# Optimization experiments

Measured on AMD Instinct MI355X. Metric: run time of the kernel, lower is better.

The kernel has to match this reference:

```python
import jax, jax.numpy as jnp
import numpy as np

N, C, H, W = 1, 1, 4096, 4096

def setup_inputs() -> dict:
    key = jax.random.key(0)
    x = jax.random.normal(key, (N, C, H, W), dtype=jnp.float32)
    return {"x": x}

def reference(x):
    # torch.median returns the lower of the two middle values for even counts:
    # take the k-th smallest with k = (n-1)//2.
    n = x.size
    median = jnp.sort(x.reshape(-1))[(n - 1) // 2]
    # threshold everything below the median to zero
    thresholded = jnp.where(x < median, jnp.float32(0.0), x)
    # 7x7 max pool, stride 1, padding 3 (torch pads with -inf for max pool)
    pooled = jax.lax.reduce_window(
        thresholded,
        -jnp.inf,
        jax.lax.max,
        window_dimensions=(1, 1, 7, 7),
        window_strides=(1, 1, 1, 1),
        padding=[(0, 0), (0, 0), (3, 3), (3, 3)],
    )
    # In the original, gather(flatten(thresholded), max_indices) == pooled,
    # so binarize where the thresholded value equals its local window max.
    binarized = jnp.where(thresholded == pooled, jnp.float32(1.0), jnp.float32(0.0))
    return binarized * x
```

## Files before the change

kernel.cpp:

```cpp
#include <hip/hip_runtime.h>
#include <math.h>

#define IMG_H 4096
#define IMG_W 4096
#define TS 64
#define HALO 3
#define TW 70
#define THS 71
#define HMS 65
#define NBINS 4096
#define CBLK 1024
#define CAPB 4096
#define WLO (-0.001953125f)
#define WHI ( 0.001953125f)
#define MCAP 1024
#define NSUB 2048

struct SelState { float median; };

__device__ __forceinline__ unsigned f2u(float f) {
    unsigned b = __float_as_uint(f);
    unsigned mask = (unsigned)(-(int)(b >> 31)) | 0x80000000u;
    return b ^ mask;
}
__device__ __forceinline__ float u2f(unsigned u) {
    unsigned mask = (u >> 31) ? 0x80000000u : 0xFFFFFFFFu;
    return __uint_as_float(u ^ mask);
}

__device__ __forceinline__ int val_bin(float v) {
    float t = (v + 4.0f) * 512.0f;
    int b = (int)t;
    b = b < 0 ? 0 : b;
    b = b > (NBINS - 1) ? (NBINS - 1) : b;
    return b;
}

__device__ __forceinline__ int sub_bin(float v) {
    float t = (v - WLO) * (float)(NSUB * 256);
    int b = (int)t;
    b = b < 0 ? 0 : b;
    b = b > (NSUB - 1) ? (NSUB - 1) : b;
    return b;
}

__global__ __launch_bounds__(512, 8) void count_compact(
    const float4* __restrict__ x4, int n4,
    unsigned* __restrict__ belowCnt,
    unsigned* __restrict__ candCnt,
    unsigned* __restrict__ candA)
{
    __shared__ unsigned buf[CAPB];
    __shared__ unsigned wred[8];
    __shared__ unsigned lcnt;
    const int t = threadIdx.x;
    if (t == 0) lcnt = 0;
    __syncthreads();

    unsigned below = 0;
    const int idx = blockIdx.x * 512 + t;
    const int stride = CBLK * 512;

    if (n4 == 8 * stride) {
        float4 v[8];
        #pragma unroll
        for (int j = 0; j < 8; j++) v[j] = x4[idx + j * stride];
        #pragma unroll
        for (int j = 0; j < 8; j++) {
            float vs[4] = {v[j].x, v[j].y, v[j].z, v[j].w};
            #pragma unroll
            for (int u = 0; u < 4; u++) {
                float vv = vs[u];
                below += (vv < WLO) ? 1u : 0u;
                if (vv >= WLO && vv < WHI) {
                    unsigned p = atomicAdd(&lcnt, 1u);
                    if (p < CAPB) buf[p] = f2u(vv);
                }
            }
        }
    } else {
        for (int i = idx; i < n4; i += stride) {
            float4 v = x4[i];
            float vs[4] = {v.x, v.y, v.z, v.w};
            #pragma unroll
            for (int u = 0; u < 4; u++) {
                float vv = vs[u];
                below += (vv < WLO) ? 1u : 0u;
                if (vv >= WLO && vv < WHI) {
                    unsigned p = atomicAdd(&lcnt, 1u);
                    if (p < CAPB) buf[p] = f2u(vv);
                }
            }
        }
    }

    #pragma unroll
    for (int off = 32; off >= 1; off >>= 1) below += __shfl_down(below, off, 64);
    if ((t & 63) == 0) wred[t >> 6] = below;
    __syncthreads();
    if (t == 0) {
        unsigned tot = 0;
        #pragma unroll
        for (int w = 0; w < 8; w++) tot += wred[w];
        belowCnt[blockIdx.x] = tot;
        candCnt[blockIdx.x] = lcnt;
    }
    unsigned m = lcnt; if (m > CAPB) m = CAPB;
    const unsigned gbase = (unsigned)blockIdx.x * CAPB;
    for (unsigned i = t; i < m; i += 512) candA[gbase + i] = buf[i];
}

__global__ __launch_bounds__(1024) void finalize_fb(
    const float4* __restrict__ x4, int n4, unsigned K,
    const unsigned* __restrict__ belowCnt,
    const unsigned* __restrict__ candCnt,
    const unsigned* __restrict__ candA,
    unsigned* __restrict__ candB,
    SelState* __restrict__ st)
{
    __shared__ unsigned hist[NSUB];
    __shared__ unsigned mem[MCAP];
    __shared__ unsigned lh[NBINS];
    __shared__ unsigned ccs[CBLK];
    __shared__ unsigned wsA[16], wsB[16], wsC[16];
    __shared__ unsigned s_below, s_M, s_ovf, s_sb, s_kr2, mcnt;
    __shared__ unsigned s_bin, s_krem, s_m, s_pref, s_kr;
    const int t = threadIdx.x;
    const unsigned lane = t & 63, wid = t >> 6;

    const unsigned rbase = wid * 64u;
    unsigned key[64];
    #pragma unroll
    for (int g = 0; g < 64; g++)
        key[g] = candA[(rbase + (unsigned)g) * CAPB + lane];

    {
        const unsigned cc = candCnt[t];
        ccs[t] = cc;
        unsigned bsum = belowCnt[t];
        unsigned csum = cc;
        unsigned osum = (cc > CAPB) ? 1u : 0u;
        #pragma unroll
        for (int off = 32; off >= 1; off >>= 1) {
            bsum += __shfl_down(bsum, off, 64);
            csum += __shfl_down(csum, off, 64);
            osum += __shfl_down(osum, off, 64);
        }
        if (lane == 0) { wsA[wid] = bsum; wsB[wid] = csum; wsC[wid] = osum; }
        if (t == 0) mcnt = 0;
        for (int i = t; i < NSUB; i += 1024) hist[i] = 0;
        __syncthreads();
        if (t == 0) {
            unsigned b = 0, c = 0, o = 0;
            #pragma unroll
            for (int w = 0; w < 16; w++) { b += wsA[w]; c += wsB[w]; o += wsC[w]; }
            s_below = b; s_M = c; s_ovf = o;
        }
        __syncthreads();
    }

    const unsigned below = s_below, M = s_M;
    bool resolved = false;
    if (s_ovf == 0u && K >= below && (K - below) < M) {
        const unsigned kRem = K - below;

        #pragma unroll
        for (int g = 0; g < 64; g++)
            if (lane < ccs[rbase + (unsigned)g])
                atomicAdd(&hist[sub_bin(u2f(key[g]))], 1u);
        for (int r = t; r < CBLK; r += 1024) {
            const unsigned cc = ccs[r];
            for (unsigned j = 64; j < cc; j++)
                atomicAdd(&hist[sub_bin(u2f(candA[(unsigned)r * CAPB + j]))], 1u);
        }
        __syncthreads();

        unsigned d0 = hist[t * 2], d1 = hist[t * 2 + 1];
        unsigned loc2 = d0 + d1;
        unsigned s2 = loc2;
        #pragma unroll
        for (int off = 1; off < 64; off <<= 1) {
            unsigned u = __shfl_up(s2, off, 64);
            if (lane >= off) s2 += u;
        }
        if (lane == 63) wsA[wid] = s2;
        __syncthreads();
        unsigned base2 = 0;
        for (unsigned w = 0; w < wid; w++) base2 += wsA[w];
        unsigned excl2 = base2 + s2 - loc2;
        if (kRem >= excl2 && kRem < excl2 + loc2) {
            if (kRem < excl2 + d0) { s_sb = (unsigned)(t * 2);     s_kr2 = kRem - excl2; }
            else                   { s_sb = (unsigned)(t * 2 + 1); s_kr2 = kRem - excl2 - d0; }
        }
        __syncthreads();

        const int sb = (int)s_sb;
        #pragma unroll
        for (int g = 0; g < 64; g++) {
            if (lane < ccs[rbase + (unsigned)g] &&
                sub_bin(u2f(key[g])) == sb) {
                unsigned p = atomicAdd(&mcnt, 1u);
                if (p < MCAP) mem[p] = key[g];
            }
        }
        for (int r = t; r < CBLK; r += 1024) {
            const unsigned cc = ccs[r];
            for (unsigned j = 64; j < cc; j++) {
                unsigned k2 = candA[(unsigned)r * CAPB + j];
                if (sub_bin(u2f(k2)) == sb) {
                    unsigned p = atomicAdd(&mcnt, 1u);
                    if (p < MCAP) mem[p] = k2;
                }
            }
        }
        __syncthreads();
        if (mcnt <= MCAP) {
            const unsigned m = mcnt, kr2 = s_kr2;
            if ((unsigned)t < m) {
                unsigned ku = mem[t], c = 0, e = 0;
                for (unsigned j = 0; j < m; j++) {
                    unsigned kj = mem[j];
                    c += (kj < ku);
                    e += (kj == ku);
                }
                if (c <= kr2 && kr2 < c + e) st->median = u2f(ku);
            }
            resolved = true;
        }
    }
    if (resolved) return;

    __syncthreads();
    for (int i = t; i < NBINS; i += 1024) lh[i] = 0;
    __syncthreads();
    for (int i = t; i < n4; i += 1024) {
        float4 v = x4[i];
        atomicAdd(&lh[val_bin(v.x)], 1u);
        atomicAdd(&lh[val_bin(v.y)], 1u);
        atomicAdd(&lh[val_bin(v.z)], 1u);
        atomicAdd(&lh[val_bin(v.w)], 1u);
    }
    __syncthreads();

    {
        unsigned cb[4];
        unsigned local = 0;
        #pragma unroll
        for (int j = 0; j < 4; j++) { cb[j] = lh[t * 4 + j]; local += cb[j]; }
        unsigned s = local;
        #pragma unroll
        for (int off = 1; off < 64; off <<= 1) {
            unsigned u = __shfl_up(s, off, 64);
            if (lane >= off) s += u;
        }
        if (lane == 63) wsA[wid] = s;
        __syncthreads();
        unsigned base = 0;
        for (unsigned w = 0; w < wid; w++) base += wsA[w];
        unsigned excl = base + s - local;
        if (K >= excl && K < excl + local) {
            unsigned cum = excl;
            #pragma unroll
            for (int j = 0; j < 4; j++) {
                if (K < cum + cb[j]) { s_bin = (unsigned)(t * 4 + j); s_krem = K - cum; break; }
                cum += cb[j];
            }
        }
        if (t == 0) s_m = 0;
        __syncthreads();
    }

    {
        const int b = (int)s_bin;
        for (int i = t; i < n4; i += 1024) {
            float4 v = x4[i];
            float vs[4] = {v.x, v.y, v.z, v.w};
            #pragma unroll
            for (int j = 0; j < 4; j++) {
                if (val_bin(vs[j]) == b) {
                    unsigned p = atomicAdd(&s_m, 1u);
                    candB[p] = f2u(vs[j]);
                }
            }
        }
        __syncthreads();
    }

    const int M2 = (int)s_m;
    if (t == 0) { s_pref = 0; s_kr = s_krem; }
    for (int p = 0; p < 3; p++) {
        const int shift = (p == 0) ? 21 : ((p == 1) ? 10 : 0);
        const int bits  = (p == 2) ? 10 : 11;
        const int nb    = 1 << bits;
        for (int i = t; i < nb; i += 1024) lh[i] = 0;
        __syncthreads();
        const unsigned pref = s_pref;
        for (int i = t; i < M2; i += 1024) {
            unsigned u = candB[i];
            bool ok = (p == 0) || ((u >> ((p == 1) ? 21 : 10)) == pref);
            if (ok) atomicAdd(&lh[(u >> shift) & (unsigned)(nb - 1)], 1u);
        }
        __syncthreads();
        const int P = nb >> 10;
        unsigned c0 = lh[t * (P ? P : 1)];
        unsigned c1 = (P == 2) ? lh[t * 2 + 1] : 0u;
        if (P == 0) { c0 = (t < nb) ? lh[t] : 0u; c1 = 0u; }
        unsigned local = c0 + c1;
        unsigned s = local;
        #pragma unroll
        for (int off = 1; off < 64; off <<= 1) {
            unsigned u = __shfl_up(s, off, 64);
            if (lane >= off) s += u;
        }
        if (lane == 63) wsA[wid] = s;
        __syncthreads();
        unsigned base = 0;
        for (unsigned w = 0; w < wid; w++) base += wsA[w];
        unsigned excl = base + s - local;
        unsigned kRem2 = s_kr;
        __syncthreads();
        if (kRem2 >= excl && kRem2 < excl + local) {
            if (P == 2) {
                if (kRem2 < excl + c0) { s_pref = (pref << bits) | (unsigned)(t * 2);     s_kr = kRem2 - excl; }
                else                  { s_pref = (pref << bits) | (unsigned)(t * 2 + 1); s_kr = kRem2 - excl - c0; }
            } else {
                s_pref = (pref << bits) | (unsigned)t;
                s_kr = kRem2 - excl;
            }
        }
        __syncthreads();
    }
    if (t == 0) st->median = u2f(s_pref);
}

__global__ __launch_bounds__(512) void nms_kernel(
    const float* __restrict__ x, float* __restrict__ out,
    const SelState* __restrict__ st)
{
    __shared__ float th[TW * THS];
    __shared__ float hm[TW * HMS];

    const float med = st->median;
    const float NEGINF = -__builtin_inff();
    const int bx = blockIdx.x, by = blockIdx.y;
    const int gy0 = by * TS - HALO;
    const int gcol0 = bx * TS - 4;

    if (bx >= 1 && bx <= (IMG_W / TS) - 2 && by >= 1 && by <= (IMG_H / TS) - 2) {
        #pragma unroll
        for (int k = 0; k < 3; k++) {
            int task = threadIdx.x + k * 512;
            if (task < TW * 18) {
                int r = task / 18, q = task - r * 18;
                const float4 v = *(const float4*)&x[(gy0 + r) * IMG_W + (gcol0 + q * 4)];
                float vs[4] = {v.x, v.y, v.z, v.w};
                #pragma unroll
                for (int cmp = 0; cmp < 4; cmp++) {
                    int c = q * 4 - 1 + cmp;
                    if ((unsigned)c < (unsigned)TW)
                        th[r * THS + c] = (vs[cmp] < med) ? 0.0f : vs[cmp];
                }
            }
        }
    } else {
        for (int task = threadIdx.x; task < TW * 18; task += 512) {
            int r = task / 18, q = task - r * 18;
            int gy = gy0 + r;
            int gxb = gcol0 + q * 4;
            bool rowok = (gy >= 0 && gy < IMG_H);
            float vs[4];
            if (rowok && gxb >= 0 && gxb + 4 <= IMG_W) {
                float4 v = *(const float4*)&x[gy * IMG_W + gxb];
                vs[0] = v.x; vs[1] = v.y; vs[2] = v.z; vs[3] = v.w;
            } else if (rowok) {
                #pragma unroll
                for (int cmp = 0; cmp < 4; cmp++) {
                    int gx = gxb + cmp;
                    vs[cmp] = (gx >= 0 && gx < IMG_W) ? x[gy * IMG_W + gx] : NEGINF;
                }
            } else {
                vs[0] = vs[1] = vs[2] = vs[3] = NEGINF;
            }
            #pragma unroll
            for (int cmp = 0; cmp < 4; cmp++) {
                int c = q * 4 - 1 + cmp;
                if ((unsigned)c < (unsigned)TW) {
                    float v = vs[cmp];
                    v = (v == NEGINF) ? v : ((v < med) ? 0.0f : v);
                    th[r * THS + c] = v;
                }
            }
        }
    }
    __syncthreads();

    for (int task = threadIdx.x; task < TW * 8; task += 512) {
        int r = task % TW;
        int c0 = (task / TW) * 8;
        float w[7];
        #pragma unroll
        for (int i = 0; i < 14; i++) {
            w[i % 7] = th[r * THS + c0 + i];
            if (i >= 6) {
                float m = w[0];
                #pragma unroll
                for (int k = 1; k < 7; k++) m = fmaxf(m, w[k]);
                hm[r * HMS + c0 + i - 6] = m;
            }
        }
    }
    __syncthreads();

    {
        const int c = threadIdx.x & 63;
        const int rr0 = (threadIdx.x >> 6) * 8;
        float w[7];
        #pragma unroll
        for (int i = 0; i < 14; i++) {
            w[i % 7] = hm[(rr0 + i) * HMS + c];
            if (i >= 6) {
                int R = rr0 + i - 6;
                float m = w[0];
                #pragma unroll
                for (int k = 1; k < 7; k++) m = fmaxf(m, w[k]);
                float t = th[(R + HALO) * THS + (c + HALO)];
                int gy = by * TS + R;
                int gx = bx * TS + c;
                float o = 0.0f;
                if (t == m) {
                    o = (t != 0.0f) ? t : x[gy * IMG_W + gx];
                }
                out[gy * IMG_W + gx] = o;
            }
        }
    }
}

extern "C" void kernel_launch(void* const* d_in, const int* in_sizes, int n_in,
                              void* d_out, int out_size, void* d_ws, size_t ws_size,
                              hipStream_t stream)
{
    const float* x = (const float*)d_in[0];
    float* out = (float*)d_out;
    const int n = in_sizes[0];
    const unsigned K = (unsigned)((n - 1) / 2);

    char* ws = (char*)d_ws;
    SelState* st       = (SelState*)ws;
    unsigned* belowCnt = (unsigned*)(ws + 1024);
    unsigned* candCnt  = (unsigned*)(ws + 1024 + 4096);
    unsigned* candA    = (unsigned*)(ws + ws_size / 2);

    const int n4 = n / 4;
    count_compact<<<CBLK, 512, 0, stream>>>((const float4*)x, n4,
                                            belowCnt, candCnt, candA);
    finalize_fb<<<1, 1024, 0, stream>>>((const float4*)x, n4, K,
                                        belowCnt, candCnt, candA,
                                        (unsigned*)d_out, st);
    dim3 fg(IMG_W / TS, IMG_H / TS);
    nms_kernel<<<fg, 512, 0, stream>>>(x, out, st);
}
```

Measured before the change: 146.6 us.

## Fuse median selection and NMS into one cooperative persistent kernel with grid syncs

Replaces the three launches (count/compact, single-block finalize, tiled NMS) with a single cooperative kernel of 512 blocks. Grid syncs separate the phases. The candidate histogram and sub-bin selection are spread across all blocks using global atomics instead of one 1024-thread block. Each block then processes 8 NMS tiles in a persistent loop. This removes the serial single-block finalize bottleneck and the launch gaps, at the cost of grid-sync overhead, fewer resident blocks for the NMS phase, and a redundant O(m^2) rank computation run in every block.

```diff
diff --git a/kernel.cpp b/kernel.cpp
--- a/kernel.cpp
+++ b/kernel.cpp
@@ -1,5 +1,8 @@
 #include <hip/hip_runtime.h>
+#include <hip/hip_cooperative_groups.h>
 #include <math.h>
+
+namespace cg = cooperative_groups;
 
 #define IMG_H 4096
 #define IMG_W 4096
@@ -9,13 +12,16 @@
 #define THS 71
 #define HMS 65
 #define NBINS 4096
-#define CBLK 1024
+#define GRIDB 512
+#define NTHR 512
 #define CAPB 4096
 #define WLO (-0.001953125f)
 #define WHI ( 0.001953125f)
 #define MCAP 1024
 #define NSUB 2048
 
+#define CBLK 1024
+
 struct SelState { float median; };
 
 __device__ __forceinline__ unsigned f2u(float f) {
@@ -27,7 +33,6 @@
     unsigned mask = (u >> 31) ? 0x80000000u : 0xFFFFFFFFu;
     return __uint_as_float(u ^ mask);
 }
-
 __device__ __forceinline__ int val_bin(float v) {
     float t = (v + 4.0f) * 512.0f;
     int b = (int)t;
@@ -35,7 +40,6 @@
     b = b > (NBINS - 1) ? (NBINS - 1) : b;
     return b;
 }
-
 __device__ __forceinline__ int sub_bin(float v) {
     float t = (v - WLO) * (float)(NSUB * 256);
     int b = (int)t;
@@ -44,10 +48,352 @@
     return b;
 }
 
+union SMem {
+    struct { unsigned buf[CAPB]; unsigned wred[8]; unsigned lcnt; } a;
+    struct { unsigned lh[NBINS];
+             unsigned s_below, s_M, s_ovf, s_sb, s_kr2, s_cnt;
+             unsigned s_bin, s_krem, s_m, s_pref, s_kr;
+             float s_med; } b;
+    struct { float th[TW * THS]; float hm[TW * HMS]; } c;
+};
+
+__global__ __launch_bounds__(NTHR, 4) void fused_nms(
+    const float4* __restrict__ x4, int n4, unsigned K,
+    const float* __restrict__ x, float* __restrict__ out,
+    unsigned* __restrict__ candB,
+    SelState* __restrict__ st,
+    unsigned* __restrict__ belowCnt,
+    unsigned* __restrict__ candCnt,
+    unsigned* __restrict__ candA,
+    unsigned* __restrict__ ghist,
+    unsigned* __restrict__ gmem,
+    unsigned* __restrict__ gmcnt, unsigned* __restrict__ gfb)
+{
+    __shared__ SMem sm;
+    cg::grid_group grid = cg::this_grid();
+    const int t = threadIdx.x;
+    const int b = blockIdx.x;
+    const unsigned lane = t & 63, wid = t >> 6;
+
+    if (t == 0) sm.a.lcnt = 0;
+    __syncthreads();
+    if (b == 0) {
+        for (int i = t; i < NSUB; i += NTHR) ghist[i] = 0;
+        if (t == 0) { *gmcnt = 0; *gfb = 0; }
+    }
+    unsigned below = 0;
+    const int gid = b * NTHR + t;
+    const int stride = GRIDB * NTHR;
+    if (n4 == 16 * stride) {
+        #pragma unroll
+        for (int half = 0; half < 2; half++) {
+            float4 v[8];
+            #pragma unroll
+            for (int j = 0; j < 8; j++) v[j] = x4[gid + (half * 8 + j) * stride];
+            #pragma unroll
+            for (int j = 0; j < 8; j++) {
+                float vs[4] = {v[j].x, v[j].y, v[j].z, v[j].w};
+                #pragma unroll
+                for (int u = 0; u < 4; u++) {
+                    float vv = vs[u];
+                    below += (vv < WLO) ? 1u : 0u;
+                    if (vv >= WLO && vv < WHI) {
+                        unsigned p = atomicAdd(&sm.a.lcnt, 1u);
+                        if (p < CAPB) sm.a.buf[p] = f2u(vv);
+                    }
+                }
+            }
+        }
+    } else {
+        for (int i = gid; i < n4; i += stride) {
+            float4 v = x4[i];
+            float vs[4] = {v.x, v.y, v.z, v.w};
+            #pragma unroll
+            for (int u = 0; u < 4; u++) {
+                float vv = vs[u];
+                below += (vv < WLO) ? 1u : 0u;
+                if (vv >= WLO && vv < WHI) {
+                    unsigned p = atomicAdd(&sm.a.lcnt, 1u);
+                    if (p < CAPB) sm.a.buf[p] = f2u(vv);
+                }
+            }
+        }
+    }
+    #pragma unroll
+    for (int off = 32; off >= 1; off >>= 1) below += __shfl_down(below, off, 64);
+    if (lane == 0) sm.a.wred[wid] = below;
+    __syncthreads();
+    if (t == 0) {
+        unsigned tot = 0;
+        #pragma unroll
+        for (int w = 0; w < 8; w++) tot += sm.a.wred[w];
+        belowCnt[b] = tot;
+        candCnt[b] = sm.a.lcnt;
+    }
+    unsigned m0 = sm.a.lcnt; if (m0 > CAPB) m0 = CAPB;
+    for (unsigned i = t; i < m0; i += NTHR) candA[(unsigned)b * CAPB + i] = sm.a.buf[i];
+    grid.sync();
+
+    {
+        const unsigned ccv = candCnt[t];
+        unsigned bsum = belowCnt[t];
+        unsigned csum = ccv;
+        unsigned osum = (ccv > CAPB) ? 1u : 0u;
+        #pragma unroll
+        for (int off = 32; off >= 1; off >>= 1) {
+            bsum += __shfl_down(bsum, off, 64);
+            csum += __shfl_down(csum, off, 64);
+            osum += __shfl_down(osum, off, 64);
+        }
+        if (lane == 0) { sm.b.lh[wid] = bsum; sm.b.lh[8 + wid] = csum; sm.b.lh[16 + wid] = osum; }
+        __syncthreads();
+        if (t == 0) {
+            unsigned bb = 0, cc = 0, oo = 0;
+            #pragma unroll
+            for (int w = 0; w < 8; w++) { bb += sm.b.lh[w]; cc += sm.b.lh[8 + w]; oo += sm.b.lh[16 + w]; }
+            sm.b.s_below = bb; sm.b.s_M = cc; sm.b.s_ovf = oo;
+        }
+        __syncthreads();
+    }
+    {
+        unsigned cc = candCnt[b]; if (cc > CAPB) cc = CAPB;
+        for (unsigned j = t; j < cc; j += NTHR)
+            atomicAdd(&ghist[sub_bin(u2f(candA[(unsigned)b * CAPB + j]))], 1u);
+    }
+    grid.sync();
+
+    const unsigned belowT = sm.b.s_below, Mtot = sm.b.s_M;
+    const bool fastok = (sm.b.s_ovf == 0u) && (K >= belowT) && (K - belowT < Mtot);
+    if (fastok) {
+        const unsigned kRem = K - belowT;
+        unsigned d[4], local = 0;
+        #pragma unroll
+        for (int j = 0; j < 4; j++) { d[j] = ghist[t * 4 + j]; local += d[j]; }
+        unsigned s = local;
+        #pragma unroll
+        for (int off = 1; off < 64; off <<= 1) {
+            unsigned u = __shfl_up(s, off, 64);
+            if (lane >= off) s += u;
+        }
+        if (lane == 63) sm.b.lh[wid] = s;
+        __syncthreads();
+        unsigned base = 0;
+        for (unsigned w = 0; w < wid; w++) base += sm.b.lh[w];
+        unsigned excl = base + s - local;
+        if (kRem >= excl && kRem < excl + local) {
+            unsigned cum = excl;
+            #pragma unroll
+            for (int j = 0; j < 4; j++) {
+                if (kRem < cum + d[j]) {
+                    sm.b.s_sb = (unsigned)(t * 4 + j);
+                    sm.b.s_kr2 = kRem - cum;
+                    sm.b.s_cnt = d[j];
+                    break;
+                }
+                cum += d[j];
+            }
+        }
+        __syncthreads();
+    }
+    bool needfb = true;
+    if (fastok) needfb = (sm.b.s_cnt > MCAP);
+    if (!needfb) {
+        unsigned cc = candCnt[b]; if (cc > CAPB) cc = CAPB;
+        const unsigned sb = sm.b.s_sb;
+        for (unsigned j = t; j < cc; j += NTHR) {
+            unsigned key = candA[(unsigned)b * CAPB + j];
+            if ((unsigned)sub_bin(u2f(key)) == sb) {
+                unsigned p = atomicAdd(gmcnt, 1u);
+                if (p < MCAP) gmem[p] = key;
+            }
+        }
+    } else if (b == 0) {
+        for (int i = t; i < NBINS; i += NTHR) sm.b.lh[i] = 0;
+        __syncthreads();
+        for (int i = t; i < n4; i += NTHR) {
+            float4 v = x4[i];
+            atomicAdd(&sm.b.lh[val_bin(v.x)], 1u);
+            atomicAdd(&sm.b.lh[val_bin(v.y)], 1u);
+            atomicAdd(&sm.b.lh[val_bin(v.z)], 1u);
+            atomicAdd(&sm.b.lh[val_bin(v.w)], 1u);
+        }
+        __syncthreads();
+        if (t == 0) {
+            unsigned cum = 0;
+            for (int i = 0; i < NBINS; i++) {
+                unsigned c = sm.b.lh[i];
+                if (K < cum + c) { sm.b.s_bin = (unsigned)i; sm.b.s_krem = K - cum; break; }
+                cum += c;
+            }
+            sm.b.s_m = 0;
+        }
+        __syncthreads();
+        {
+            const unsigned bin = sm.b.s_bin;
+            for (int i = t; i < n4; i += NTHR) {
+                float4 v = x4[i];
+                float vs[4] = {v.x, v.y, v.z, v.w};
+                #pragma unroll
+                for (int j = 0; j < 4; j++) {
+                    if ((unsigned)val_bin(vs[j]) == bin) {
+                        unsigned p = atomicAdd(&sm.b.s_m, 1u);
+                        candB[p] = f2u(vs[j]);
+                    }
+                }
+            }
+            __syncthreads();
+        }
+        const int M2 = (int)sm.b.s_m;
+        if (t == 0) { sm.b.s_pref = 0; sm.b.s_kr = sm.b.s_krem; }
+        __syncthreads();
+        for (int p = 0; p < 3; p++) {
+            const int shift = (p == 0) ? 21 : ((p == 1) ? 10 : 0);
+            const int bits  = (p == 2) ? 10 : 11;
+            const int nb    = 1 << bits;
+            for (int i = t; i < nb; i += NTHR) sm.b.lh[i] = 0;
+            __syncthreads();
+            const unsigned pref = sm.b.s_pref;
+            for (int i = t; i < M2; i += NTHR) {
+                unsigned u = candB[i];
+                bool ok = (p == 0) || ((u >> ((p == 1) ? 21 : 10)) == pref);
+                if (ok) atomicAdd(&sm.b.lh[(u >> shift) & (unsigned)(nb - 1)], 1u);
+            }
+            __syncthreads();
+            if (t == 0) {
+                unsigned kr = sm.b.s_kr, cum = 0;
+                for (int i = 0; i < nb; i++) {
+                    unsigned c = sm.b.lh[i];
+                    if (kr < cum + c) { sm.b.s_pref = (pref << bits) | (unsigned)i; sm.b.s_kr = kr - cum; break; }
+                    cum += c;
+                }
+            }
+            __syncthreads();
+        }
+        if (t == 0) { st->median = u2f(sm.b.s_pref); *gfb = 1u; }
+    }
+    grid.sync();
+
+    float med;
+    if (*gfb) {
+        med = st->median;
+    } else {
+        const unsigned m = *gmcnt;
+        const unsigned kr2 = sm.b.s_kr2;
+        for (unsigned tt = t; tt < m; tt += NTHR) {
+            unsigned ku = gmem[tt], c = 0, e = 0;
+            for (unsigned j = 0; j < m; j++) {
+                unsigned kj = gmem[j];
+                c += (kj < ku);
+                e += (kj == ku);
+            }
+            if (c <= kr2 && kr2 < c + e) sm.b.s_med = u2f(ku);
+        }
+        __syncthreads();
+        med = sm.b.s_med;
+    }
+
+    const float NEGINF = -__builtin_inff();
+    for (int it = 0; it < 8; ++it) {
+        __syncthreads();
+        const int tile = b * 8 + it;
+        const int bx = tile & 63, by = tile >> 6;
+        const int gy0 = by * TS - HALO;
+        const int gcol0 = bx * TS - 4;
+
+        if (bx >= 1 && bx <= 62 && by >= 1 && by <= 62) {
+            #pragma unroll
+            for (int k = 0; k < 3; k++) {
+                int task = t + k * NTHR;
+                if (task < TW * 18) {
+                    int r = task / 18, q = task - r * 18;
+                    const float4 v = *(const float4*)&x[(gy0 + r) * IMG_W + (gcol0 + q * 4)];
+                    float vs[4] = {v.x, v.y, v.z, v.w};
+                    #pragma unroll
+                    for (int cmp = 0; cmp < 4; cmp++) {
+                        int c = q * 4 - 1 + cmp;
+                        if ((unsigned)c < (unsigned)TW)
+                            sm.c.th[r * THS + c] = (vs[cmp] < med) ? 0.0f : vs[cmp];
+                    }
+                }
+            }
+        } else {
+            for (int task = t; task < TW * 18; task += NTHR) {
+                int r = task / 18, q = task - r * 18;
+                int gy = gy0 + r;
+                int gxb = gcol0 + q * 4;
+                bool rowok = (gy >= 0 && gy < IMG_H);
+                float vs[4];
+                if (rowok && gxb >= 0 && gxb + 4 <= IMG_W) {
+                    float4 v = *(const float4*)&x[gy * IMG_W + gxb];
+                    vs[0] = v.x; vs[1] = v.y; vs[2] = v.z; vs[3] = v.w;
+                } else if (rowok) {
+                    #pragma unroll
+                    for (int cmp = 0; cmp < 4; cmp++) {
+                        int gx = gxb + cmp;
+                        vs[cmp] = (gx >= 0 && gx < IMG_W) ? x[gy * IMG_W + gx] : NEGINF;
+                    }
+                } else {
+                    vs[0] = vs[1] = vs[2] = vs[3] = NEGINF;
+                }
+                #pragma unroll
+                for (int cmp = 0; cmp < 4; cmp++) {
+                    int c = q * 4 - 1 + cmp;
+                    if ((unsigned)c < (unsigned)TW) {
+                        float v = vs[cmp];
+                        v = (v == NEGINF) ? v : ((v < med) ? 0.0f : v);
+                        sm.c.th[r * THS + c] = v;
+                    }
+                }
+            }
+        }
+        __syncthreads();
+
+        for (int task = t; task < TW * 8; task += NTHR) {
+            int r = task % TW;
+            int c0 = (task / TW) * 8;
+            float w[7];
+            #pragma unroll
+            for (int i = 0; i < 14; i++) {
+                w[i % 7] = sm.c.th[r * THS + c0 + i];
+                if (i >= 6) {
+                    float m = w[0];
+                    #pragma unroll
+                    for (int k = 1; k < 7; k++) m = fmaxf(m, w[k]);
+                    sm.c.hm[r * HMS + c0 + i - 6] = m;
+                }
+            }
+        }
+        __syncthreads();
+
+        {
+            const int c = t & 63;
+            const int rr0 = (t >> 6) * 8;
+            float w[7];
+            #pragma unroll
+            for (int i = 0; i < 14; i++) {
+                w[i % 7] = sm.c.hm[(rr0 + i) * HMS + c];
+                if (i >= 6) {
+                    int R = rr0 + i - 6;
+                    float m = w[0];
+                    #pragma unroll
+                    for (int k = 1; k < 7; k++) m = fmaxf(m, w[k]);
+                    float tv = sm.c.th[(R + HALO) * THS + (c + HALO)];
+                    int gy = by * TS + R;
+                    int gx = bx * TS + c;
+                    float o = 0.0f;
+                    if (tv == m) {
+                        o = (tv != 0.0f) ? tv : x[gy * IMG_W + gx];
+                    }
+                    out[gy * IMG_W + gx] = o;
+                }
+            }
+        }
+    }
+}
+
 __global__ __launch_bounds__(512, 8) void count_compact(
     const float4* __restrict__ x4, int n4,
-    unsigned* __restrict__ belowCnt,
-    unsigned* __restrict__ candCnt,
+    unsigned* __restrict__ belowCnt, unsigned* __restrict__ candCnt,
     unsigned* __restrict__ candA)
 {
     __shared__ unsigned buf[CAPB];
@@ -56,44 +402,22 @@
     const int t = threadIdx.x;
     if (t == 0) lcnt = 0;
     __syncthreads();
-
     unsigned below = 0;
     const int idx = blockIdx.x * 512 + t;
     const int stride = CBLK * 512;
-
-    if (n4 == 8 * stride) {
-        float4 v[8];
-        #pragma unroll
-        for (int j = 0; j < 8; j++) v[j] = x4[idx + j * stride];
-        #pragma unroll
-        for (int j = 0; j < 8; j++) {
-            float vs[4] = {v[j].x, v[j].y, v[j].z, v[j].w};
-            #pragma unroll
-            for (int u = 0; u < 4; u++) {
-                float vv = vs[u];
-                below += (vv < WLO) ? 1u : 0u;
-                if (vv >= WLO && vv < WHI) {
-                    unsigned p = atomicAdd(&lcnt, 1u);
-                    if (p < CAPB) buf[p] = f2u(vv);
-                }
-            }
-        }
-    } else {
-        for (int i = idx; i < n4; i += stride) {
-            float4 v = x4[i];
-            float vs[4] = {v.x, v.y, v.z, v.w};
-            #pragma unroll
-            for (int u = 0; u < 4; u++) {
-                float vv = vs[u];
-                below += (vv < WLO) ? 1u : 0u;
-                if (vv >= WLO && vv < WHI) {
-                    unsigned p = atomicAdd(&lcnt, 1u);
-                    if (p < CAPB) buf[p] = f2u(vv);
-                }
-            }
-        }
-    }
-
+    for (int i = idx; i < n4; i += stride) {
+        float4 v = x4[i];
+        float vs[4] = {v.x, v.y, v.z, v.w};
+        #pragma unroll
+        for (int u = 0; u < 4; u++) {
+            float vv = vs[u];
+            below += (vv < WLO) ? 1u : 0u;
+            if (vv >= WLO && vv < WHI) {
+                unsigned p = atomicAdd(&lcnt, 1u);
+                if (p < CAPB) buf[p] = f2u(vv);
+            }
+        }
+    }
     #pragma unroll
     for (int off = 32; off >= 1; off >>= 1) below += __shfl_down(below, off, 64);
     if ((t & 63) == 0) wred[t >> 6] = below;
@@ -112,10 +436,8 @@
 
 __global__ __launch_bounds__(1024) void finalize_fb(
     const float4* __restrict__ x4, int n4, unsigned K,
-    const unsigned* __restrict__ belowCnt,
-    const unsigned* __restrict__ candCnt,
-    const unsigned* __restrict__ candA,
-    unsigned* __restrict__ candB,
+    const unsigned* __restrict__ belowCnt, const unsigned* __restrict__ candCnt,
+    const unsigned* __restrict__ candA, unsigned* __restrict__ candB,
     SelState* __restrict__ st)
 {
     __shared__ unsigned hist[NSUB];
@@ -127,13 +449,11 @@
     __shared__ unsigned s_bin, s_krem, s_m, s_pref, s_kr;
     const int t = threadIdx.x;
     const unsigned lane = t & 63, wid = t >> 6;
-
     const unsigned rbase = wid * 64u;
     unsigned key[64];
     #pragma unroll
     for (int g = 0; g < 64; g++)
         key[g] = candA[(rbase + (unsigned)g) * CAPB + lane];
-
     {
         const unsigned cc = candCnt[t];
         ccs[t] = cc;
@@ -151,19 +471,17 @@
         for (int i = t; i < NSUB; i += 1024) hist[i] = 0;
         __syncthreads();
         if (t == 0) {
-            unsigned b = 0, c = 0, o = 0;
-            #pragma unroll
-            for (int w = 0; w < 16; w++) { b += wsA[w]; c += wsB[w]; o += wsC[w]; }
-            s_below = b; s_M = c; s_ovf = o;
-        }
-        __syncthreads();
-    }
-
+            unsigned bb = 0, cc2 = 0, oo = 0;
+            #pragma unroll
+            for (int w = 0; w < 16; w++) { bb += wsA[w]; cc2 += wsB[w]; oo += wsC[w]; }
+            s_below = bb; s_M = cc2; s_ovf = oo;
+        }
+        __syncthreads();
+    }
     const unsigned below = s_below, M = s_M;
     bool resolved = false;
     if (s_ovf == 0u && K >= below && (K - below) < M) {
         const unsigned kRem = K - below;
-
         #pragma unroll
         for (int g = 0; g < 64; g++)
             if (lane < ccs[rbase + (unsigned)g])
@@ -174,7 +492,6 @@
                 atomicAdd(&hist[sub_bin(u2f(candA[(unsigned)r * CAPB + j]))], 1u);
         }
         __syncthreads();
-
         unsigned d0 = hist[t * 2], d1 = hist[t * 2 + 1];
         unsigned loc2 = d0 + d1;
         unsigned s2 = loc2;
@@ -193,12 +510,10 @@
             else                   { s_sb = (unsigned)(t * 2 + 1); s_kr2 = kRem - excl2 - d0; }
         }
         __syncthreads();
-
         const int sb = (int)s_sb;
         #pragma unroll
         for (int g = 0; g < 64; g++) {
-            if (lane < ccs[rbase + (unsigned)g] &&
-                sub_bin(u2f(key[g])) == sb) {
+            if (lane < ccs[rbase + (unsigned)g] && sub_bin(u2f(key[g])) == sb) {
                 unsigned p = atomicAdd(&mcnt, 1u);
                 if (p < MCAP) mem[p] = key[g];
             }
@@ -229,7 +544,6 @@
         }
     }
     if (resolved) return;
-
     __syncthreads();
     for (int i = t; i < NBINS; i += 1024) lh[i] = 0;
     __syncthreads();
@@ -241,7 +555,6 @@
         atomicAdd(&lh[val_bin(v.w)], 1u);
     }
     __syncthreads();
-
     {
         unsigned cb[4];
         unsigned local = 0;
@@ -269,15 +582,14 @@
         if (t == 0) s_m = 0;
         __syncthreads();
     }
-
     {
-        const int b = (int)s_bin;
+        const int bb = (int)s_bin;
         for (int i = t; i < n4; i += 1024) {
             float4 v = x4[i];
             float vs[4] = {v.x, v.y, v.z, v.w};
             #pragma unroll
             for (int j = 0; j < 4; j++) {
-                if (val_bin(vs[j]) == b) {
+                if (val_bin(vs[j]) == bb) {
                     unsigned p = atomicAdd(&s_m, 1u);
                     candB[p] = f2u(vs[j]);
                 }
@@ -285,7 +597,6 @@
         }
         __syncthreads();
     }
-
     const int M2 = (int)s_m;
     if (t == 0) { s_pref = 0; s_kr = s_krem; }
     for (int p = 0; p < 3; p++) {
@@ -322,7 +633,7 @@
         if (kRem2 >= excl && kRem2 < excl + local) {
             if (P == 2) {
                 if (kRem2 < excl + c0) { s_pref = (pref << bits) | (unsigned)(t * 2);     s_kr = kRem2 - excl; }
-                else                  { s_pref = (pref << bits) | (unsigned)(t * 2 + 1); s_kr = kRem2 - excl - c0; }
+                else                   { s_pref = (pref << bits) | (unsigned)(t * 2 + 1); s_kr = kRem2 - excl - c0; }
             } else {
                 s_pref = (pref << bits) | (unsigned)t;
                 s_kr = kRem2 - excl;
@@ -339,14 +650,12 @@
 {
     __shared__ float th[TW * THS];
     __shared__ float hm[TW * HMS];
-
     const float med = st->median;
     const float NEGINF = -__builtin_inff();
     const int bx = blockIdx.x, by = blockIdx.y;
     const int gy0 = by * TS - HALO;
     const int gcol0 = bx * TS - 4;
-
-    if (bx >= 1 && bx <= (IMG_W / TS) - 2 && by >= 1 && by <= (IMG_H / TS) - 2) {
+    if (bx >= 1 && bx <= 62 && by >= 1 && by <= 62) {
         #pragma unroll
         for (int k = 0; k < 3; k++) {
             int task = threadIdx.x + k * 512;
@@ -393,7 +702,6 @@
         }
     }
     __syncthreads();
-
     for (int task = threadIdx.x; task < TW * 8; task += 512) {
         int r = task % TW;
         int c0 = (task / TW) * 8;
@@ -410,7 +718,6 @@
         }
     }
     __syncthreads();
-
     {
         const int c = threadIdx.x & 63;
         const int rr0 = (threadIdx.x >> 6) * 8;
@@ -423,12 +730,12 @@
                 float m = w[0];
                 #pragma unroll
                 for (int k = 1; k < 7; k++) m = fmaxf(m, w[k]);
-                float t = th[(R + HALO) * THS + (c + HALO)];
+                float tv = th[(R + HALO) * THS + (c + HALO)];
                 int gy = by * TS + R;
                 int gx = bx * TS + c;
                 float o = 0.0f;
-                if (t == m) {
-                    o = (t != 0.0f) ? t : x[gy * IMG_W + gx];
+                if (tv == m) {
+                    o = (tv != 0.0f) ? tv : x[gy * IMG_W + gx];
                 }
                 out[gy * IMG_W + gx] = o;
             }
@@ -444,19 +751,34 @@
     float* out = (float*)d_out;
     const int n = in_sizes[0];
     const unsigned K = (unsigned)((n - 1) / 2);
-
     char* ws = (char*)d_ws;
+
     SelState* st       = (SelState*)ws;
-    unsigned* belowCnt = (unsigned*)(ws + 1024);
-    unsigned* candCnt  = (unsigned*)(ws + 1024 + 4096);
+    unsigned* gfb      = (unsigned*)(ws + 64);
+    unsigned* gmcnt    = (unsigned*)(ws + 128);
+    unsigned* ghist    = (unsigned*)(ws + 256);
+    unsigned* belowCnt = (unsigned*)(ws + 16384);
+    unsigned* candCnt  = (unsigned*)(ws + 24576);
+    unsigned* gmem     = (unsigned*)(ws + 32768);
     unsigned* candA    = (unsigned*)(ws + ws_size / 2);
 
-    const int n4 = n / 4;
-    count_compact<<<CBLK, 512, 0, stream>>>((const float4*)x, n4,
-                                            belowCnt, candCnt, candA);
-    finalize_fb<<<1, 1024, 0, stream>>>((const float4*)x, n4, K,
-                                        belowCnt, candCnt, candA,
-                                        (unsigned*)d_out, st);
-    dim3 fg(IMG_W / TS, IMG_H / TS);
-    nms_kernel<<<fg, 512, 0, stream>>>(x, out, st);
-}
+    const float4* x4 = (const float4*)x;
+    unsigned* candB = (unsigned*)d_out;
+    int n4 = n / 4;
+    unsigned Kv = K;
+
+    void* args[] = { (void*)&x4, (void*)&n4, (void*)&Kv, (void*)&x, (void*)&out,
+                     (void*)&candB, (void*)&st, (void*)&belowCnt, (void*)&candCnt,
+                     (void*)&candA, (void*)&ghist, (void*)&gmem, (void*)&gmcnt,
+                     (void*)&gfb };
+    hipError_t err = hipLaunchCooperativeKernel((void*)fused_nms,
+                                                dim3(GRIDB), dim3(NTHR),
+                                                args, 0, stream);
+    if (err != hipSuccess) {
+        count_compact<<<CBLK, 512, 0, stream>>>(x4, n4, belowCnt, candCnt, candA);
+        finalize_fb<<<1, 1024, 0, stream>>>(x4, n4, K, belowCnt, candCnt, candA,
+                                            candB, st);
+        dim3 fg(IMG_W / TS, IMG_H / TS);
+        nms_kernel<<<fg, 512, 0, stream>>>(x, out, st);
+    }
+}
```

Result: slower. 319.9 us (+118.2%).

## Fuse median counting and finalize into one kernel via last-block election

Applied to the files above, without the earlier changes.

Merges the count/compact kernel and the single-block finalize kernel into one launch. Each block increments a global done counter after a threadfence, and the last block to arrive runs the median selection with 512 threads instead of 1024. This removes one kernel launch and the gap between launches, but adds a memset launch. The heavy shared-memory footprint (about 45KB per block) and the halved thread count in the finalize phase may lower occupancy in the count phase and slow the selection.

```diff
diff --git a/kernel.cpp b/kernel.cpp
--- a/kernel.cpp
+++ b/kernel.cpp
@@ -27,7 +27,6 @@
     unsigned mask = (u >> 31) ? 0x80000000u : 0xFFFFFFFFu;
     return __uint_as_float(u ^ mask);
 }
-
 __device__ __forceinline__ int val_bin(float v) {
     float t = (v + 4.0f) * 512.0f;
     int b = (int)t;
@@ -35,7 +34,6 @@
     b = b > (NBINS - 1) ? (NBINS - 1) : b;
     return b;
 }
-
 __device__ __forceinline__ int sub_bin(float v) {
     float t = (v - WLO) * (float)(NSUB * 256);
     int b = (int)t;
@@ -44,23 +42,32 @@
     return b;
 }
 
-__global__ __launch_bounds__(512, 8) void count_compact(
-    const float4* __restrict__ x4, int n4,
+__global__ __launch_bounds__(512, 4) void count_finalize(
+    const float4* __restrict__ x4, int n4, unsigned K,
     unsigned* __restrict__ belowCnt,
     unsigned* __restrict__ candCnt,
-    unsigned* __restrict__ candA)
+    unsigned* __restrict__ candA,
+    unsigned* __restrict__ candB,
+    SelState* __restrict__ st,
+    unsigned* __restrict__ done)
 {
     __shared__ unsigned buf[CAPB];
-    __shared__ unsigned wred[8];
-    __shared__ unsigned lcnt;
+    __shared__ unsigned hist[NSUB];
+    __shared__ unsigned mem[MCAP];
+    __shared__ unsigned lh[NBINS];
+    __shared__ unsigned ccs[CBLK];
+    __shared__ unsigned wsA[8], wsB[8], wsC[8], wred[8];
+    __shared__ unsigned lcnt, s_lastflag;
+    __shared__ unsigned s_below, s_M, s_ovf, s_sb, s_kr2, mcnt;
+    __shared__ unsigned s_bin, s_krem, s_m, s_pref, s_kr;
     const int t = threadIdx.x;
+    const unsigned lane = t & 63, wid = t >> 6;
+
     if (t == 0) lcnt = 0;
     __syncthreads();
-
     unsigned below = 0;
     const int idx = blockIdx.x * 512 + t;
     const int stride = CBLK * 512;
-
     if (n4 == 8 * stride) {
         float4 v[8];
         #pragma unroll
@@ -93,10 +100,9 @@
             }
         }
     }
-
     #pragma unroll
     for (int off = 32; off >= 1; off >>= 1) below += __shfl_down(below, off, 64);
-    if ((t & 63) == 0) wred[t >> 6] = below;
+    if (lane == 0) wred[wid] = below;
     __syncthreads();
     if (t == 0) {
         unsigned tot = 0;
@@ -105,41 +111,26 @@
         belowCnt[blockIdx.x] = tot;
         candCnt[blockIdx.x] = lcnt;
     }
-    unsigned m = lcnt; if (m > CAPB) m = CAPB;
+    unsigned m0 = lcnt; if (m0 > CAPB) m0 = CAPB;
     const unsigned gbase = (unsigned)blockIdx.x * CAPB;
-    for (unsigned i = t; i < m; i += 512) candA[gbase + i] = buf[i];
-}
-
-__global__ __launch_bounds__(1024) void finalize_fb(
-    const float4* __restrict__ x4, int n4, unsigned K,
-    const unsigned* __restrict__ belowCnt,
-    const unsigned* __restrict__ candCnt,
-    const unsigned* __restrict__ candA,
-    unsigned* __restrict__ candB,
-    SelState* __restrict__ st)
-{
-    __shared__ unsigned hist[NSUB];
-    __shared__ unsigned mem[MCAP];
-    __shared__ unsigned lh[NBINS];
-    __shared__ unsigned ccs[CBLK];
-    __shared__ unsigned wsA[16], wsB[16], wsC[16];
-    __shared__ unsigned s_below, s_M, s_ovf, s_sb, s_kr2, mcnt;
-    __shared__ unsigned s_bin, s_krem, s_m, s_pref, s_kr;
-    const int t = threadIdx.x;
-    const unsigned lane = t & 63, wid = t >> 6;
-
-    const unsigned rbase = wid * 64u;
-    unsigned key[64];
-    #pragma unroll
-    for (int g = 0; g < 64; g++)
-        key[g] = candA[(rbase + (unsigned)g) * CAPB + lane];
+    for (unsigned i = t; i < m0; i += 512) candA[gbase + i] = buf[i];
+
+    __threadfence();
+    __syncthreads();
+    if (t == 0) {
+        unsigned prev = atomicAdd(done, 1u);
+        s_lastflag = (prev == (unsigned)(CBLK - 1)) ? 1u : 0u;
+    }
+    __syncthreads();
+    if (!s_lastflag) return;
+    __threadfence();
 
     {
-        const unsigned cc = candCnt[t];
-        ccs[t] = cc;
-        unsigned bsum = belowCnt[t];
-        unsigned csum = cc;
-        unsigned osum = (cc > CAPB) ? 1u : 0u;
+        const unsigned c0 = candCnt[t], c1 = candCnt[t + 512];
+        ccs[t] = c0; ccs[t + 512] = c1;
+        unsigned bsum = belowCnt[t] + belowCnt[t + 512];
+        unsigned csum = c0 + c1;
+        unsigned osum = ((c0 > CAPB) ? 1u : 0u) + ((c1 > CAPB) ? 1u : 0u);
         #pragma unroll
         for (int off = 32; off >= 1; off >>= 1) {
             bsum += __shfl_down(bsum, off, 64);
@@ -148,66 +139,87 @@
         }
         if (lane == 0) { wsA[wid] = bsum; wsB[wid] = csum; wsC[wid] = osum; }
         if (t == 0) mcnt = 0;
-        for (int i = t; i < NSUB; i += 1024) hist[i] = 0;
+        for (int i = t; i < NSUB; i += 512) hist[i] = 0;
         __syncthreads();
         if (t == 0) {
-            unsigned b = 0, c = 0, o = 0;
-            #pragma unroll
-            for (int w = 0; w < 16; w++) { b += wsA[w]; c += wsB[w]; o += wsC[w]; }
-            s_below = b; s_M = c; s_ovf = o;
-        }
-        __syncthreads();
-    }
-
-    const unsigned below = s_below, M = s_M;
+            unsigned bb = 0, cc = 0, oo = 0;
+            #pragma unroll
+            for (int w = 0; w < 8; w++) { bb += wsA[w]; cc += wsB[w]; oo += wsC[w]; }
+            s_below = bb; s_M = cc; s_ovf = oo;
+        }
+        __syncthreads();
+    }
+
+    const unsigned belowT = s_below, M = s_M;
     bool resolved = false;
-    if (s_ovf == 0u && K >= below && (K - below) < M) {
-        const unsigned kRem = K - below;
-
-        #pragma unroll
-        for (int g = 0; g < 64; g++)
-            if (lane < ccs[rbase + (unsigned)g])
-                atomicAdd(&hist[sub_bin(u2f(key[g]))], 1u);
-        for (int r = t; r < CBLK; r += 1024) {
+    if (s_ovf == 0u && K >= belowT && (K - belowT) < M) {
+        const unsigned kRem = K - belowT;
+
+        #pragma unroll
+        for (int half = 0; half < 2; half++) {
+            const unsigned rbase = (unsigned)half * 512u + wid * 64u;
+            unsigned key[64];
+            #pragma unroll
+            for (int g = 0; g < 64; g++)
+                key[g] = candA[(rbase + (unsigned)g) * CAPB + lane];
+            #pragma unroll
+            for (int g = 0; g < 64; g++)
+                if (lane < ccs[rbase + (unsigned)g])
+                    atomicAdd(&hist[sub_bin(u2f(key[g]))], 1u);
+        }
+        for (int r = t; r < CBLK; r += 512) {
             const unsigned cc = ccs[r];
             for (unsigned j = 64; j < cc; j++)
                 atomicAdd(&hist[sub_bin(u2f(candA[(unsigned)r * CAPB + j]))], 1u);
         }
         __syncthreads();
 
-        unsigned d0 = hist[t * 2], d1 = hist[t * 2 + 1];
-        unsigned loc2 = d0 + d1;
-        unsigned s2 = loc2;
+        unsigned d[4], local = 0;
+        #pragma unroll
+        for (int j = 0; j < 4; j++) { d[j] = hist[t * 4 + j]; local += d[j]; }
+        unsigned s = local;
         #pragma unroll
         for (int off = 1; off < 64; off <<= 1) {
-            unsigned u = __shfl_up(s2, off, 64);
-            if (lane >= off) s2 += u;
-        }
-        if (lane == 63) wsA[wid] = s2;
-        __syncthreads();
-        unsigned base2 = 0;
-        for (unsigned w = 0; w < wid; w++) base2 += wsA[w];
-        unsigned excl2 = base2 + s2 - loc2;
-        if (kRem >= excl2 && kRem < excl2 + loc2) {
-            if (kRem < excl2 + d0) { s_sb = (unsigned)(t * 2);     s_kr2 = kRem - excl2; }
-            else                   { s_sb = (unsigned)(t * 2 + 1); s_kr2 = kRem - excl2 - d0; }
-        }
-        __syncthreads();
-
-        const int sb = (int)s_sb;
-        #pragma unroll
-        for (int g = 0; g < 64; g++) {
-            if (lane < ccs[rbase + (unsigned)g] &&
-                sub_bin(u2f(key[g])) == sb) {
-                unsigned p = atomicAdd(&mcnt, 1u);
-                if (p < MCAP) mem[p] = key[g];
-            }
-        }
-        for (int r = t; r < CBLK; r += 1024) {
+            unsigned u = __shfl_up(s, off, 64);
+            if (lane >= off) s += u;
+        }
+        if (lane == 63) wsA[wid] = s;
+        __syncthreads();
+        unsigned base = 0;
+        for (unsigned w = 0; w < wid; w++) base += wsA[w];
+        unsigned excl = base + s - local;
+        if (kRem >= excl && kRem < excl + local) {
+            unsigned cum = excl;
+            #pragma unroll
+            for (int j = 0; j < 4; j++) {
+                if (kRem < cum + d[j]) { s_sb = (unsigned)(t * 4 + j); s_kr2 = kRem - cum; break; }
+                cum += d[j];
+            }
+        }
+        __syncthreads();
+
+        const unsigned sb = s_sb;
+        #pragma unroll
+        for (int half = 0; half < 2; half++) {
+            const unsigned rbase = (unsigned)half * 512u + wid * 64u;
+            unsigned key[64];
+            #pragma unroll
+            for (int g = 0; g < 64; g++)
+                key[g] = candA[(rbase + (unsigned)g) * CAPB + lane];
+            #pragma unroll
+            for (int g = 0; g < 64; g++) {
+                if (lane < ccs[rbase + (unsigned)g] &&
+                    (unsigned)sub_bin(u2f(key[g])) == sb) {
+                    unsigned p = atomicAdd(&mcnt, 1u);
+                    if (p < MCAP) mem[p] = key[g];
+                }
+            }
+        }
+        for (int r = t; r < CBLK; r += 512) {
             const unsigned cc = ccs[r];
             for (unsigned j = 64; j < cc; j++) {
                 unsigned k2 = candA[(unsigned)r * CAPB + j];
-                if (sub_bin(u2f(k2)) == sb) {
+                if ((unsigned)sub_bin(u2f(k2)) == sb) {
                     unsigned p = atomicAdd(&mcnt, 1u);
                     if (p < MCAP) mem[p] = k2;
                 }
@@ -231,9 +243,9 @@
     if (resolved) return;
 
     __syncthreads();
-    for (int i = t; i < NBINS; i += 1024) lh[i] = 0;
-    __syncthreads();
-    for (int i = t; i < n4; i += 1024) {
+    for (int i = t; i < NBINS; i += 512) lh[i] = 0;
+    __syncthreads();
+    for (int i = t; i < n4; i += 512) {
         float4 v = x4[i];
         atomicAdd(&lh[val_bin(v.x)], 1u);
         atomicAdd(&lh[val_bin(v.y)], 1u);
@@ -241,43 +253,24 @@
         atomicAdd(&lh[val_bin(v.w)], 1u);
     }
     __syncthreads();
-
+    if (t == 0) {
+        unsigned cum = 0;
+        for (int i = 0; i < NBINS; i++) {
+            unsigned c = lh[i];
+            if (K < cum + c) { s_bin = (unsigned)i; s_krem = K - cum; break; }
+            cum += c;
+        }
+        s_m = 0;
+    }
+    __syncthreads();
     {
-        unsigned cb[4];
-        unsigned local = 0;
-        #pragma unroll
-        for (int j = 0; j < 4; j++) { cb[j] = lh[t * 4 + j]; local += cb[j]; }
-        unsigned s = local;
-        #pragma unroll
-        for (int off = 1; off < 64; off <<= 1) {
-            unsigned u = __shfl_up(s, off, 64);
-            if (lane >= off) s += u;
-        }
-        if (lane == 63) wsA[wid] = s;
-        __syncthreads();
-        unsigned base = 0;
-        for (unsigned w = 0; w < wid; w++) base += wsA[w];
-        unsigned excl = base + s - local;
-        if (K >= excl && K < excl + local) {
-            unsigned cum = excl;
-            #pragma unroll
-            for (int j = 0; j < 4; j++) {
-                if (K < cum + cb[j]) { s_bin = (unsigned)(t * 4 + j); s_krem = K - cum; break; }
-                cum += cb[j];
-            }
-        }
-        if (t == 0) s_m = 0;
-        __syncthreads();
-    }
-
-    {
-        const int b = (int)s_bin;
-        for (int i = t; i < n4; i += 1024) {
+        const unsigned bin = s_bin;
+        for (int i = t; i < n4; i += 512) {
             float4 v = x4[i];
             float vs[4] = {v.x, v.y, v.z, v.w};
             #pragma unroll
             for (int j = 0; j < 4; j++) {
-                if (val_bin(vs[j]) == b) {
+                if ((unsigned)val_bin(vs[j]) == bin) {
                     unsigned p = atomicAdd(&s_m, 1u);
                     candB[p] = f2u(vs[j]);
                 }
@@ -285,47 +278,28 @@
         }
         __syncthreads();
     }
-
     const int M2 = (int)s_m;
     if (t == 0) { s_pref = 0; s_kr = s_krem; }
+    __syncthreads();
     for (int p = 0; p < 3; p++) {
         const int shift = (p == 0) ? 21 : ((p == 1) ? 10 : 0);
         const int bits  = (p == 2) ? 10 : 11;
         const int nb    = 1 << bits;
-        for (int i = t; i < nb; i += 1024) lh[i] = 0;
+        for (int i = t; i < nb; i += 512) lh[i] = 0;
         __syncthreads();
         const unsigned pref = s_pref;
-        for (int i = t; i < M2; i += 1024) {
+        for (int i = t; i < M2; i += 512) {
             unsigned u = candB[i];
             bool ok = (p == 0) || ((u >> ((p == 1) ? 21 : 10)) == pref);
             if (ok) atomicAdd(&lh[(u >> shift) & (unsigned)(nb - 1)], 1u);
         }
         __syncthreads();
-        const int P = nb >> 10;
-        unsigned c0 = lh[t * (P ? P : 1)];
-        unsigned c1 = (P == 2) ? lh[t * 2 + 1] : 0u;
-        if (P == 0) { c0 = (t < nb) ? lh[t] : 0u; c1 = 0u; }
-        unsigned local = c0 + c1;
-        unsigned s = local;
-        #pragma unroll
-        for (int off = 1; off < 64; off <<= 1) {
-            unsigned u = __shfl_up(s, off, 64);
-            if (lane >= off) s += u;
-        }
-        if (lane == 63) wsA[wid] = s;
-        __syncthreads();
-        unsigned base = 0;
-        for (unsigned w = 0; w < wid; w++) base += wsA[w];
-        unsigned excl = base + s - local;
-        unsigned kRem2 = s_kr;
-        __syncthreads();
-        if (kRem2 >= excl && kRem2 < excl + local) {
-            if (P == 2) {
-                if (kRem2 < excl + c0) { s_pref = (pref << bits) | (unsigned)(t * 2);     s_kr = kRem2 - excl; }
-                else                  { s_pref = (pref << bits) | (unsigned)(t * 2 + 1); s_kr = kRem2 - excl - c0; }
-            } else {
-                s_pref = (pref << bits) | (unsigned)t;
-                s_kr = kRem2 - excl;
+        if (t == 0) {
+            unsigned kr = s_kr, cum = 0;
+            for (int i = 0; i < nb; i++) {
+                unsigned c = lh[i];
+                if (kr < cum + c) { s_pref = (pref << bits) | (unsigned)i; s_kr = kr - cum; break; }
+                cum += c;
             }
         }
         __syncthreads();
@@ -346,7 +320,7 @@
     const int gy0 = by * TS - HALO;
     const int gcol0 = bx * TS - 4;
 
-    if (bx >= 1 && bx <= (IMG_W / TS) - 2 && by >= 1 && by <= (IMG_H / TS) - 2) {
+    if (bx >= 1 && bx <= 62 && by >= 1 && by <= 62) {
         #pragma unroll
         for (int k = 0; k < 3; k++) {
             int task = threadIdx.x + k * 512;
@@ -423,12 +397,12 @@
                 float m = w[0];
                 #pragma unroll
                 for (int k = 1; k < 7; k++) m = fmaxf(m, w[k]);
-                float t = th[(R + HALO) * THS + (c + HALO)];
+                float tv = th[(R + HALO) * THS + (c + HALO)];
                 int gy = by * TS + R;
                 int gx = bx * TS + c;
                 float o = 0.0f;
-                if (t == m) {
-                    o = (t != 0.0f) ? t : x[gy * IMG_W + gx];
+                if (tv == m) {
+                    o = (tv != 0.0f) ? tv : x[gy * IMG_W + gx];
                 }
                 out[gy * IMG_W + gx] = o;
             }
@@ -447,16 +421,16 @@
 
     char* ws = (char*)d_ws;
     SelState* st       = (SelState*)ws;
-    unsigned* belowCnt = (unsigned*)(ws + 1024);
-    unsigned* candCnt  = (unsigned*)(ws + 1024 + 4096);
+    unsigned* done     = (unsigned*)(ws + 64);
+    unsigned* belowCnt = (unsigned*)(ws + 16384);
+    unsigned* candCnt  = (unsigned*)(ws + 24576);
     unsigned* candA    = (unsigned*)(ws + ws_size / 2);
 
     const int n4 = n / 4;
-    count_compact<<<CBLK, 512, 0, stream>>>((const float4*)x, n4,
-                                            belowCnt, candCnt, candA);
-    finalize_fb<<<1, 1024, 0, stream>>>((const float4*)x, n4, K,
-                                        belowCnt, candCnt, candA,
-                                        (unsigned*)d_out, st);
+    hipMemsetAsync(done, 0, 4, stream);
+    count_finalize<<<CBLK, 512, 0, stream>>>((const float4*)x, n4, K,
+                                             belowCnt, candCnt, candA,
+                                             (unsigned*)d_out, st, done);
     dim3 fg(IMG_W / TS, IMG_H / TS);
     nms_kernel<<<fg, 512, 0, stream>>>(x, out, st);
 }
```

New measurement: 383.9 us. 2.62x slower.
